# Performance work log

Hardware: AMD Instinct MI355X
Metric: run time of the kernel (lower is better)

## Reference

```python
import math
import jax, jax.numpy as jnp
import numpy as np

N_LAYERS = 30
RC = 64        # residual_channels
N_MELS = 80
TED = 128      # time_emb_dim
CD = 256       # text_dim
B, T = 8, 8192
EPS = 1e-12    # F.normalize eps


def conv1d(x, w, b, dilation=1, padding=0):
    # x: [B,C,T], w: [O,I,K], b: [O]
    y = jax.lax.conv_general_dilated(
        x, w, window_strides=(1,), padding=[(padding, padding)],
        rhs_dilation=(dilation,), dimension_numbers=("NCH", "OIH", "NCH"))
    return y + b[None, :, None]


def sinusoidal_embedding(t, dim):
    half = dim // 2
    freqs = jnp.exp(jnp.arange(half, dtype=jnp.float32) * (-math.log(10000.0) / (half - 1)))
    ang = t.astype(jnp.float32)[:, None] * freqs[None, :]
    return jnp.concatenate([jnp.sin(ang), jnp.cos(ang)], axis=1)  # [B, dim]


def mish(x):
    return x * jnp.tanh(jax.nn.softplus(x))


def setup_inputs() -> dict:
    key = jax.random.key(0)
    ks = jax.random.split(key, 24)
    s = 0.05
    inp = {
        "x": jax.random.normal(ks[0], (B, 1, N_MELS, T), jnp.float32),
        "t": jax.random.randint(ks[1], (B,), 0, 1000),
        "c_emb": jax.random.normal(ks[2], (B, CD), jnp.float32),
        # input_proj: Conv1d(n_mels, RC, 1)
        "in_w": jax.random.normal(ks[3], (RC, N_MELS, 1), jnp.float32) * s,
        "in_b": jnp.zeros((RC,), jnp.float32),
        # time MLP: Linear(TED, 4*TED), Mish, Linear(4*TED, TED). torch weight [out,in]
        "te_w1": jax.random.normal(ks[4], (4 * TED, TED), jnp.float32) * s,
        "te_b1": jnp.zeros((4 * TED,), jnp.float32),
        "te_w2": jax.random.normal(ks[5], (TED, 4 * TED), jnp.float32) * s,
        "te_b2": jnp.zeros((TED,), jnp.float32),
        # per-layer stacked params
        "dconv_w": jax.random.normal(ks[6], (N_LAYERS, 2 * RC, RC, 3), jnp.float32) * s,
        "dconv_b": jnp.zeros((N_LAYERS, 2 * RC), jnp.float32),
        "tproj_w": jax.random.normal(ks[7], (N_LAYERS, 2 * RC, TED), jnp.float32) * s,
        "tproj_b": jnp.zeros((N_LAYERS, 2 * RC), jnp.float32),
        "cproj_w": jax.random.normal(ks[8], (N_LAYERS, 2 * RC, CD), jnp.float32) * s,
        "cproj_b": jnp.zeros((N_LAYERS, 2 * RC), jnp.float32),
        "rs_w": jax.random.normal(ks[9], (N_LAYERS, 2 * RC, RC, 1), jnp.float32) * s,
        "rs_b": jnp.zeros((N_LAYERS, 2 * RC), jnp.float32),
        "skip_w": jax.random.normal(ks[10], (RC, RC, 1), jnp.float32) * s,
        "skip_b": jnp.zeros((RC,), jnp.float32),
        "out_w": jax.random.normal(ks[11], (N_MELS, RC, 1), jnp.float32) * s,
        "out_b": jnp.zeros((N_MELS,), jnp.float32),
    }
    return inp


def reference(x, t, c_emb, in_w, in_b, te_w1, te_b1, te_w2, te_b2,
              dconv_w, dconv_b, tproj_w, tproj_b, cproj_w, cproj_b,
              rs_w, rs_b, skip_w, skip_b, out_w, out_b):
    h = x[:, 0]                                  # squeeze(1) -> [B, n_mels, T]
    h = conv1d(h, in_w, in_b)                    # [B, RC, T]
    te = sinusoidal_embedding(t, TED)
    te = mish(te @ te_w1.T + te_b1) @ te_w2.T + te_b2   # [B, TED]

    skips = jnp.zeros_like(conv1d(h, rs_w[0], rs_b[0])[:, :RC])  # [B, RC, T]
    skips = jnp.zeros((h.shape[0], RC, h.shape[2]), h.dtype)
    for i in range(N_LAYERS):
        dil = 2 ** (i % 10)
        g = conv1d(h, dconv_w[i], dconv_b[i], dilation=dil, padding=dil)  # [B, 2RC, T]
        tp = (te @ tproj_w[i].T + tproj_b[i])[:, :, None]                 # [B, 2RC, 1]
        tp = tp / jnp.maximum(jnp.abs(tp), EPS)      # F.normalize over size-1 dim
        cp = (c_emb @ cproj_w[i].T + cproj_b[i])[:, :, None]
        cp = cp / jnp.maximum(jnp.abs(cp), EPS)
        g = g + tp + cp
        gate, filt = g[:, :RC], g[:, RC:]            # chunk(2, dim=1)
        out = jnp.tanh(filt) * jax.nn.sigmoid(gate)
        rs = conv1d(out, rs_w[i], rs_b[i])           # [B, 2RC, T]
        res, skip = rs[:, :RC], rs[:, RC:]
        h = h + res * (1.0 / math.sqrt(2.0))
        skips = skips + skip

    y = skips / math.sqrt(N_LAYERS)
    y = jax.nn.relu(conv1d(y, skip_w, skip_b))
    y = conv1d(y, out_w, out_b)                      # [B, n_mels, T]
    return y[:, None]                                # unsqueeze(1)
```

## Files before the change

kernel.cpp:

```cpp
#include <hip/hip_runtime.h>
#include <hip/hip_bf16.h>
#include <math.h>

#define NL 30
#define NM 80
#define Bx 8
#define Tx 8192

typedef short short8 __attribute__((ext_vector_type(8)));
typedef float f32x4 __attribute__((ext_vector_type(4)));
typedef unsigned int u32x2 __attribute__((ext_vector_type(2)));
typedef unsigned int u32x4 __attribute__((ext_vector_type(4)));

__device__ __forceinline__ float bf2f(unsigned short u) {
    union { unsigned int u; float f; } v; v.u = ((unsigned int)u) << 16; return v.f;
}
__device__ __forceinline__ unsigned short f2bf(float f) {
    union { float f; unsigned int u; } v; v.f = f;
    unsigned int r = v.u + 0x7FFFu + ((v.u >> 16) & 1u);
    return (unsigned short)(r >> 16);
}

#if defined(__has_builtin)
#if __has_builtin(__builtin_amdgcn_global_load_lds)
#define HAS_GLL 1
#endif
#endif

__device__ __forceinline__ void gll16(const void* g, void* l) {
#ifdef HAS_GLL
    __builtin_amdgcn_global_load_lds(
        (const __attribute__((address_space(1))) void*)g,
        (__attribute__((address_space(3))) void*)l, 16, 0, 0);
#else
    int lane = threadIdx.x & 63;
    *(u32x4*)((char*)l + lane * 16) = *(const u32x4*)((const char*)g + lane * 16);
#endif
}

__global__ __launch_bounds__(512) void setup_kernel(
        const float* __restrict__ dconv_w, const float* __restrict__ rs_w,
        const float* __restrict__ skip_w, const float* __restrict__ out_w,
        unsigned short* __restrict__ wc2, unsigned short* __restrict__ wr2,
        unsigned short* __restrict__ skw16, unsigned short* __restrict__ oww16,
        const float* __restrict__ x, const float* __restrict__ in_w,
        const float* __restrict__ in_b, unsigned short* __restrict__ h0) {
    __shared__ __align__(16) unsigned char smem[49152];
    int blk = blockIdx.x;
    int tid = threadIdx.x;
    if (blk < 30) {
        int l = blk;
        unsigned short* st = (unsigned short*)smem;
        const f32x4* src4 = (const f32x4*)(dconv_w + (size_t)l * 24576);
        #pragma unroll
        for (int h = 0; h < 2; ++h) {
            f32x4 v[6];
            #pragma unroll
            for (int it = 0; it < 6; ++it)
                v[it] = src4[(h * 6 + it) * 512 + tid];
            #pragma unroll
            for (int it = 0; it < 6; ++it) {
                int chunk = (h * 6 + it) * 512 + tid;
                #pragma unroll
                for (int e = 0; e < 4; ++e) {
                    int sidx = chunk * 4 + e;
                    int oc = sidx / 192;
                    int r = sidx - oc * 192;
                    int ic = r / 3;
                    int tap = r - ic * 3;
                    int dst = tap * 8192 + oc * 64 + (((ic >> 3) ^ (oc & 7)) << 3) + (ic & 7);
                    st[dst] = f2bf(v[it][e]);
                }
            }
        }
        __syncthreads();
        u32x4* dst4 = (u32x4*)(wc2 + (size_t)l * 24576);
        const u32x4* s4 = (const u32x4*)st;
        #pragma unroll
        for (int it = 0; it < 6; ++it)
            dst4[it * 512 + tid] = s4[it * 512 + tid];
    } else if (blk < 60) {
        int l = blk - 30;
        unsigned short* st = (unsigned short*)smem;
        const f32x4* src4 = (const f32x4*)(rs_w + (size_t)l * 8192);
        f32x4 v[4];
        #pragma unroll
        for (int it = 0; it < 4; ++it)
            v[it] = src4[it * 512 + tid];
        #pragma unroll
        for (int it = 0; it < 4; ++it) {
            int chunk = it * 512 + tid;
            #pragma unroll
            for (int e = 0; e < 4; ++e) {
                int sidx = chunk * 4 + e;
                int row = sidx >> 6;
                int ic = sidx & 63;
                int dst = row * 64 + (((ic >> 3) ^ (row & 7)) << 3) + (ic & 7);
                st[dst] = f2bf(v[it][e]);
            }
        }
        __syncthreads();
        u32x4* dst4 = (u32x4*)(wr2 + (size_t)l * 8192);
        const u32x4* s4 = (const u32x4*)st;
        #pragma unroll
        for (int it = 0; it < 2; ++it)
            dst4[it * 512 + tid] = s4[it * 512 + tid];
    } else if (blk == 60) {
        for (int j = tid; j < 4096; j += 512)
            skw16[j] = f2bf(skip_w[j] * 0.18257418583505536f);
        for (int j = tid; j < 5120; j += 512)
            oww16[j] = f2bf(out_w[j]);
    } else {
        float (*wT)[64] = (float(*)[64])smem;
        for (int i = tid; i < NM * 64; i += 512) {
            int m = i >> 6, c = i & 63;
            wT[m][c] = in_w[c * NM + m];
        }
        __syncthreads();
        int j = blk - 61;
        int b = j >> 5;
        int t = (j & 31) * 256 + (tid >> 1);
        int ch0 = (tid & 1) * 32;
        const float* xp = x + (size_t)b * NM * Tx + t;
        float acc[32];
        #pragma unroll
        for (int c = 0; c < 32; ++c) acc[c] = in_b[ch0 + c];
        #pragma unroll 1
        for (int m0 = 0; m0 < NM; m0 += 8) {
            float xv[8];
            #pragma unroll
            for (int u = 0; u < 8; ++u) xv[u] = xp[(size_t)(m0 + u) * Tx];
            #pragma unroll
            for (int u = 0; u < 8; ++u) {
                #pragma unroll
                for (int c = 0; c < 32; ++c)
                    acc[c] = fmaf(xv[u], wT[m0 + u][ch0 + c], acc[c]);
            }
        }
        unsigned short* hp = h0 + ((size_t)b * Tx + t) * 64 + ch0;
        #pragma unroll
        for (int c = 0; c < 32; c += 2) {
            unsigned int p = (unsigned int)f2bf(acc[c]) | ((unsigned int)f2bf(acc[c + 1]) << 16);
            *(unsigned int*)(hp + c) = p;
        }
    }
}

__global__ __launch_bounds__(512) void gbias_kernel(
        const int* __restrict__ tin,
        const float* __restrict__ w1, const float* __restrict__ b1,
        const float* __restrict__ w2, const float* __restrict__ b2,
        const float* __restrict__ cemb,
        const float* __restrict__ tpw, const float* __restrict__ tpb,
        const float* __restrict__ cpw, const float* __restrict__ cpb,
        const float* __restrict__ dcb,
        float* __restrict__ gbias) {
    __shared__ float emb[128];
    __shared__ float h1s[512];
    __shared__ float red[512];
    __shared__ float ted[128];
    int l = blockIdx.x >> 3;
    int b = blockIdx.x & 7;
    int tid = threadIdx.x, wid = tid >> 6, lane = tid & 63;

    if (tid < 64) {
        float fr = expf(-(float)tid * (logf(10000.f) / 63.f));
        float ang = (float)tin[b] * fr;
        emb[tid] = sinf(ang);
        emb[tid + 64] = cosf(ang);
    }
    __syncthreads();
    {
        float a = b1[tid];
        const f32x4* wr4 = (const f32x4*)(w1 + tid * 128);
        #pragma unroll 8
        for (int k = 0; k < 32; ++k) {
            f32x4 w4 = wr4[k];
            a = fmaf(emb[k * 4], w4[0], a);
            a = fmaf(emb[k * 4 + 1], w4[1], a);
            a = fmaf(emb[k * 4 + 2], w4[2], a);
            a = fmaf(emb[k * 4 + 3], w4[3], a);
        }
        float sp = (a > 15.f) ? a : log1pf(expf(a));
        h1s[tid] = a * tanhf(sp);
    }
    __syncthreads();
    {
        int o = tid & 127, q = tid >> 7;
        float p = 0.f;
        const f32x4* wr4 = (const f32x4*)(w2 + o * 512 + q * 128);
        const float* hq = h1s + q * 128;
        #pragma unroll 8
        for (int k = 0; k < 32; ++k) {
            f32x4 w4 = wr4[k];
            p = fmaf(hq[k * 4], w4[0], p);
            p = fmaf(hq[k * 4 + 1], w4[1], p);
            p = fmaf(hq[k * 4 + 2], w4[2], p);
            p = fmaf(hq[k * 4 + 3], w4[3], p);
        }
        red[tid] = p;
    }
    __syncthreads();
    if (tid < 128)
        ted[tid] = b2[tid] + red[tid] + red[tid + 128] + red[tid + 256] + red[tid + 384];
    __syncthreads();

    float te0 = ted[lane];
    float te1 = ted[64 + lane];
    float ce0 = cemb[b * 256 + lane];
    float ce1 = cemb[b * 256 + 64 + lane];
    float ce2 = cemb[b * 256 + 128 + lane];
    float ce3 = cemb[b * 256 + 192 + lane];
    #pragma unroll 4
    for (int i = 0; i < 16; ++i) {
        int ch = i * 8 + wid;
        const float* wr = tpw + (size_t)(l * 128 + ch) * 128;
        float s = te0 * wr[lane] + te1 * wr[lane + 64];
        const float* wc = cpw + (size_t)(l * 128 + ch) * 256;
        float sc = ce0 * wc[lane] + ce1 * wc[lane + 64] + ce2 * wc[lane + 128] + ce3 * wc[lane + 192];
        #pragma unroll
        for (int off = 32; off >= 1; off >>= 1) {
            s += __shfl_xor(s, off, 64);
            sc += __shfl_xor(sc, off, 64);
        }
        if (lane == 0) {
            float tp = tpb[l * 128 + ch] + s;
            float cp = cpb[l * 128 + ch] + sc;
            float s1 = tp / fmaxf(fabsf(tp), 1e-12f);
            float s2 = cp / fmaxf(fabsf(cp), 1e-12f);
            gbias[(l * 8 + b) * 128 + ch] = dcb[l * 128 + ch] + s1 + s2;
        }
    }
}

__launch_bounds__(512, 4)
__global__ void layer_kernel(const unsigned short* __restrict__ h_in,
                             unsigned short* __restrict__ h_out,
                             float* __restrict__ skips,
                             const unsigned short* __restrict__ wc2,
                             const unsigned short* __restrict__ wr2,
                             const float* __restrict__ gbias,
                             const float* __restrict__ rsb,
                             int dil, int first) {
    __shared__ __align__(16) unsigned char lds[81920];
    unsigned char* ldsA = lds;
    unsigned char* ldsR = lds + 49152;
    unsigned char* ldsO = lds + 65536;

    int tid = threadIdx.x;
    int wid = tid >> 6, lane = tid & 63, lr = lane & 15, lq = lane >> 4;

    #pragma unroll
    for (int j = 0; j < 6; ++j) {
        int cbase = j * 512 + wid * 64;
        gll16(wc2 + (size_t)(cbase + lane) * 8, ldsA + cbase * 16);
    }
    #pragma unroll
    for (int j = 0; j < 2; ++j) {
        int cbase = j * 512 + wid * 64;
        gll16(wr2 + (size_t)(cbase + lane) * 8, ldsR + cbase * 16);
    }

    int bid = blockIdx.x;
    int wg = (bid & 7) * 64 + (bid >> 3);
    int b = wg >> 6;
    int t0 = ((wg & 63) << 7) + wid * 16;

    const unsigned short* hb = h_in + (size_t)b * Tx * 64;
    short8 bv[3][2];
    #pragma unroll
    for (int tap = 0; tap < 3; ++tap) {
        int toff = (tap - 1) * dil;
        int t = t0 + lr + toff;
        bool v = ((unsigned)t < (unsigned)Tx);
        #pragma unroll
        for (int kc = 0; kc < 2; ++kc) {
            short8 z = {0, 0, 0, 0, 0, 0, 0, 0};
            if (v) z = *(const short8*)(hb + t * 64 + kc * 32 + lq * 8);
            bv[tap][kc] = z;
        }
    }

    f32x4 acc[8];
    #pragma unroll
    for (int mf = 0; mf < 8; ++mf)
        acc[mf] = *(const f32x4*)(gbias + b * 128 + mf * 16 + lq * 4);
    __syncthreads();

    #pragma unroll
    for (int tap = 0; tap < 3; ++tap) {
        #pragma unroll
        for (int kc = 0; kc < 2; ++kc) {
            #pragma unroll
            for (int mf = 0; mf < 8; ++mf) {
                int row = tap * 128 + mf * 16 + lr;
                short8 af = *(const short8*)(ldsA + row * 128 + ((kc * 64 + lq * 16) ^ ((lr & 7) << 4)));
                acc[mf] = __builtin_amdgcn_mfma_f32_16x16x32_bf16(af, bv[tap][kc], acc[mf], 0, 0, 0);
            }
        }
    }

    size_t base = ((size_t)b * Tx + t0 + lr) * 64;
    u32x2 hv[4];
    f32x4 sko[4];
    #pragma unroll
    for (int mf = 0; mf < 4; ++mf) {
        hv[mf] = *(const u32x2*)(h_in + base + mf * 16 + lq * 4);
        if (!first) sko[mf] = *(const f32x4*)(skips + base + mf * 16 + lq * 4);
        else { sko[mf][0] = 0.f; sko[mf][1] = 0.f; sko[mf][2] = 0.f; sko[mf][3] = 0.f; }
    }

    unsigned char* myO = ldsO + wid * 2048;
    #pragma unroll
    for (int mf = 0; mf < 4; ++mf) {
        int p = lr;
        unsigned short ob[4];
        #pragma unroll
        for (int r = 0; r < 4; ++r) {
            float g = acc[mf][r];
            float f = acc[mf + 4][r];
            f = fminf(f, 15.f);
            g = fminf(g, 30.f);
            float ea = __builtin_amdgcn_exp2f(f * 2.8853900817779268f);
            float eb = __builtin_amdgcn_exp2f(g * 1.4426950408889634f);
            float num = (ea - 1.f) * eb;
            float den = (ea + 1.f) * (1.f + eb);
            ob[r] = f2bf(num * __builtin_amdgcn_rcpf(den));
        }
        u32x2 pk;
        pk[0] = (unsigned int)ob[0] | ((unsigned int)ob[1] << 16);
        pk[1] = (unsigned int)ob[2] | ((unsigned int)ob[3] << 16);
        *(u32x2*)(myO + p * 128 + ((mf * 32 + lq * 8) ^ ((p & 7) << 4))) = pk;
    }

    const float rt2 = 1.41421356237309505f;
    f32x4 racc[8];
    #pragma unroll
    for (int mf = 0; mf < 4; ++mf) {
        f32x4 rb = *(const f32x4*)(rsb + mf * 16 + lq * 4);
        unsigned short* hp = (unsigned short*)&hv[mf];
        f32x4 r;
        #pragma unroll
        for (int r_ = 0; r_ < 4; ++r_) r[r_] = fmaf(bf2f(hp[r_]), rt2, rb[r_]);
        racc[mf] = r;
    }
    #pragma unroll
    for (int mf = 0; mf < 4; ++mf)
        racc[mf + 4] = *(const f32x4*)(rsb + 64 + mf * 16 + lq * 4) + sko[mf];

    #pragma unroll
    for (int kc = 0; kc < 2; ++kc) {
        int p = lr;
        short8 ov = *(const short8*)(myO + p * 128 + ((kc * 64 + lq * 16) ^ ((p & 7) << 4)));
        #pragma unroll
        for (int mf = 0; mf < 8; ++mf) {
            int row = mf * 16 + lr;
            short8 af = *(const short8*)(ldsR + row * 128 + ((kc * 64 + lq * 16) ^ ((lr & 7) << 4)));
            racc[mf] = __builtin_amdgcn_mfma_f32_16x16x32_bf16(af, ov, racc[mf], 0, 0, 0);
        }
    }

    const float inv_s2 = 0.70710678118654752f;
    #pragma unroll
    for (int mf = 0; mf < 4; ++mf) {
        unsigned short hnew[4];
        #pragma unroll
        for (int r = 0; r < 4; ++r)
            hnew[r] = f2bf(racc[mf][r] * inv_s2);
        u32x2 hw;
        hw[0] = (unsigned int)hnew[0] | ((unsigned int)hnew[1] << 16);
        hw[1] = (unsigned int)hnew[2] | ((unsigned int)hnew[3] << 16);
        *(u32x2*)(h_out + base + mf * 16 + lq * 4) = hw;
        *(f32x4*)(skips + base + mf * 16 + lq * 4) = racc[mf + 4];
    }
}

__launch_bounds__(512, 2)
__global__ void layer_last_kernel(const unsigned short* __restrict__ h_in,
                                  const float* __restrict__ skips,
                                  const unsigned short* __restrict__ wc2,
                                  const unsigned short* __restrict__ wr2,
                                  const float* __restrict__ gbias,
                                  const float* __restrict__ rsb,
                                  const unsigned short* __restrict__ skw,
                                  const float* __restrict__ skb,
                                  const unsigned short* __restrict__ oww,
                                  const float* __restrict__ obias,
                                  float* __restrict__ y,
                                  int dil) {
    __shared__ __align__(16) unsigned char lds[81920];
    unsigned char* ldsA = lds;
    unsigned char* ldsR = lds + 49152;
    unsigned char* ldsO = lds + 65536;

    int tid = threadIdx.x;
    int wid = tid >> 6, lane = tid & 63, lr = lane & 15, lq = lane >> 4;

    #pragma unroll
    for (int j = 0; j < 6; ++j) {
        int cbase = j * 512 + wid * 64;
        gll16(wc2 + (size_t)(cbase + lane) * 8, ldsA + cbase * 16);
    }
    #pragma unroll
    for (int j = 0; j < 2; ++j) {
        int cbase = j * 512 + wid * 64;
        gll16(wr2 + (size_t)(cbase + lane) * 8, ldsR + cbase * 16);
    }

    int bid = blockIdx.x;
    int wg = (bid & 7) * 64 + (bid >> 3);
    int b = wg >> 6;
    int t0 = ((wg & 63) << 7) + wid * 16;

    const unsigned short* hb = h_in + (size_t)b * Tx * 64;
    short8 bv[3][2];
    #pragma unroll
    for (int tap = 0; tap < 3; ++tap) {
        int toff = (tap - 1) * dil;
        int t = t0 + lr + toff;
        bool v = ((unsigned)t < (unsigned)Tx);
        #pragma unroll
        for (int kc = 0; kc < 2; ++kc) {
            short8 z = {0, 0, 0, 0, 0, 0, 0, 0};
            if (v) z = *(const short8*)(hb + t * 64 + kc * 32 + lq * 8);
            bv[tap][kc] = z;
        }
    }

    f32x4 acc[8];
    #pragma unroll
    for (int mf = 0; mf < 8; ++mf)
        acc[mf] = *(const f32x4*)(gbias + b * 128 + mf * 16 + lq * 4);
    __syncthreads();

    #pragma unroll
    for (int tap = 0; tap < 3; ++tap) {
        #pragma unroll
        for (int kc = 0; kc < 2; ++kc) {
            #pragma unroll
            for (int mf = 0; mf < 8; ++mf) {
                int row = tap * 128 + mf * 16 + lr;
                short8 af = *(const short8*)(ldsA + row * 128 + ((kc * 64 + lq * 16) ^ ((lr & 7) << 4)));
                acc[mf] = __builtin_amdgcn_mfma_f32_16x16x32_bf16(af, bv[tap][kc], acc[mf], 0, 0, 0);
            }
        }
    }

    size_t base = ((size_t)b * Tx + t0 + lr) * 64;
    f32x4 sko[4];
    #pragma unroll
    for (int mf = 0; mf < 4; ++mf)
        sko[mf] = *(const f32x4*)(skips + base + mf * 16 + lq * 4);

    unsigned char* myO = ldsO + wid * 2048;
    #pragma unroll
    for (int mf = 0; mf < 4; ++mf) {
        int p = lr;
        unsigned short ob[4];
        #pragma unroll
        for (int r = 0; r < 4; ++r) {
            float g = acc[mf][r];
            float f = acc[mf + 4][r];
            f = fminf(f, 15.f);
            g = fminf(g, 30.f);
            float ea = __builtin_amdgcn_exp2f(f * 2.8853900817779268f);
            float eb = __builtin_amdgcn_exp2f(g * 1.4426950408889634f);
            float num = (ea - 1.f) * eb;
            float den = (ea + 1.f) * (1.f + eb);
            ob[r] = f2bf(num * __builtin_amdgcn_rcpf(den));
        }
        u32x2 pk;
        pk[0] = (unsigned int)ob[0] | ((unsigned int)ob[1] << 16);
        pk[1] = (unsigned int)ob[2] | ((unsigned int)ob[3] << 16);
        *(u32x2*)(myO + p * 128 + ((mf * 32 + lq * 8) ^ ((p & 7) << 4))) = pk;
    }

    f32x4 racc[4];
    #pragma unroll
    for (int mf = 0; mf < 4; ++mf)
        racc[mf] = *(const f32x4*)(rsb + 64 + mf * 16 + lq * 4) + sko[mf];
    #pragma unroll
    for (int kc = 0; kc < 2; ++kc) {
        int p = lr;
        short8 ov = *(const short8*)(myO + p * 128 + ((kc * 64 + lq * 16) ^ ((p & 7) << 4)));
        #pragma unroll
        for (int mf = 0; mf < 4; ++mf) {
            int row = 64 + mf * 16 + lr;
            short8 af = *(const short8*)(ldsR + row * 128 + ((kc * 64 + lq * 16) ^ ((lr & 7) << 4)));
            racc[mf] = __builtin_amdgcn_mfma_f32_16x16x32_bf16(af, ov, racc[mf], 0, 0, 0);
        }
    }

    #pragma unroll
    for (int mf = 0; mf < 4; ++mf) {
        int p = lr;
        u32x2 pk;
        pk[0] = (unsigned int)f2bf(racc[mf][0]) | ((unsigned int)f2bf(racc[mf][1]) << 16);
        pk[1] = (unsigned int)f2bf(racc[mf][2]) | ((unsigned int)f2bf(racc[mf][3]) << 16);
        *(u32x2*)(myO + p * 128 + ((mf * 32 + lq * 8) ^ ((p & 7) << 4))) = pk;
    }

    f32x4 yacc[4];
    #pragma unroll
    for (int mf = 0; mf < 4; ++mf)
        yacc[mf] = *(const f32x4*)(skb + mf * 16 + lq * 4);
    #pragma unroll
    for (int kc = 0; kc < 2; ++kc) {
        int p = lr;
        short8 Bv = *(const short8*)(myO + p * 128 + ((kc * 64 + lq * 16) ^ ((p & 7) << 4)));
        #pragma unroll
        for (int mf = 0; mf < 4; ++mf) {
            short8 A1 = *(const short8*)(skw + (mf * 16 + lr) * 64 + kc * 32 + lq * 8);
            yacc[mf] = __builtin_amdgcn_mfma_f32_16x16x32_bf16(A1, Bv, yacc[mf], 0, 0, 0);
        }
    }
    #pragma unroll
    for (int mf = 0; mf < 4; ++mf) {
        int p = lr;
        u32x2 pk;
        pk[0] = (unsigned int)f2bf(fmaxf(yacc[mf][0], 0.f)) | ((unsigned int)f2bf(fmaxf(yacc[mf][1], 0.f)) << 16);
        pk[1] = (unsigned int)f2bf(fmaxf(yacc[mf][2], 0.f)) | ((unsigned int)f2bf(fmaxf(yacc[mf][3], 0.f)) << 16);
        *(u32x2*)(myO + p * 128 + ((mf * 32 + lq * 8) ^ ((p & 7) << 4))) = pk;
    }

    f32x4 oacc[5];
    #pragma unroll
    for (int mf = 0; mf < 5; ++mf)
        oacc[mf] = *(const f32x4*)(obias + mf * 16 + lq * 4);
    #pragma unroll
    for (int kc = 0; kc < 2; ++kc) {
        int p = lr;
        short8 B2 = *(const short8*)(myO + p * 128 + ((kc * 64 + lq * 16) ^ ((p & 7) << 4)));
        #pragma unroll
        for (int mf = 0; mf < 5; ++mf) {
            short8 A2 = *(const short8*)(oww + (mf * 16 + lr) * 64 + kc * 32 + lq * 8);
            oacc[mf] = __builtin_amdgcn_mfma_f32_16x16x32_bf16(A2, B2, oacc[mf], 0, 0, 0);
        }
    }
    int t = t0 + lr;
    #pragma unroll
    for (int mf = 0; mf < 5; ++mf) {
        #pragma unroll
        for (int r = 0; r < 4; ++r) {
            int m = mf * 16 + lq * 4 + r;
            y[((size_t)b * NM + m) * Tx + t] = oacc[mf][r];
        }
    }
}

extern "C" void kernel_launch(void* const* d_in, const int* in_sizes, int n_in,
                              void* d_out, int out_size, void* d_ws, size_t ws_size,
                              hipStream_t stream) {
    const float* x       = (const float*)d_in[0];
    const int*   tin     = (const int*)d_in[1];
    const float* c_emb   = (const float*)d_in[2];
    const float* in_w    = (const float*)d_in[3];
    const float* in_b    = (const float*)d_in[4];
    const float* te_w1   = (const float*)d_in[5];
    const float* te_b1   = (const float*)d_in[6];
    const float* te_w2   = (const float*)d_in[7];
    const float* te_b2   = (const float*)d_in[8];
    const float* dconv_w = (const float*)d_in[9];
    const float* dconv_b = (const float*)d_in[10];
    const float* tproj_w = (const float*)d_in[11];
    const float* tproj_b = (const float*)d_in[12];
    const float* cproj_w = (const float*)d_in[13];
    const float* cproj_b = (const float*)d_in[14];
    const float* rs_w    = (const float*)d_in[15];
    const float* rs_b    = (const float*)d_in[16];
    const float* skip_w  = (const float*)d_in[17];
    const float* skip_b  = (const float*)d_in[18];
    const float* out_w   = (const float*)d_in[19];
    const float* out_b   = (const float*)d_in[20];

    char* ws = (char*)d_ws;
    float* gbias          = (float*)(ws + 4096);
    unsigned short* skw16 = (unsigned short*)(ws + 126976);
    unsigned short* oww16 = (unsigned short*)(ws + 135168);
    unsigned short* wc2   = (unsigned short*)(ws + 145408);
    unsigned short* wr2   = (unsigned short*)(ws + 1619968);
    unsigned short* h0    = (unsigned short*)(ws + 2111488);
    unsigned short* h1    = (unsigned short*)(ws + 10500096);
    float* skips          = (float*)(ws + 18888704);

    setup_kernel<<<317, 512, 0, stream>>>(dconv_w, rs_w, skip_w, out_w,
                                          wc2, wr2, skw16, oww16,
                                          x, in_w, in_b, h0);
    gbias_kernel<<<240, 512, 0, stream>>>(tin, te_w1, te_b1, te_w2, te_b2,
                                          c_emb, tproj_w, tproj_b,
                                          cproj_w, cproj_b, dconv_b, gbias);

    unsigned short* hin = h0;
    unsigned short* hout = h1;
    for (int i = 0; i < NL - 1; ++i) {
        int dil = 1 << (i % 10);
        layer_kernel<<<512, 512, 0, stream>>>(hin, hout, skips,
                                              wc2 + (size_t)i * 24576,
                                              wr2 + (size_t)i * 8192,
                                              gbias + (size_t)i * 1024,
                                              rs_b + (size_t)i * 128,
                                              dil, i == 0 ? 1 : 0);
        unsigned short* tmp = hin; hin = hout; hout = tmp;
    }
    layer_last_kernel<<<512, 512, 0, stream>>>(hin, skips,
                                               wc2 + (size_t)(NL - 1) * 24576,
                                               wr2 + (size_t)(NL - 1) * 8192,
                                               gbias + (size_t)(NL - 1) * 1024,
                                               rs_b + (size_t)(NL - 1) * 128,
                                               skw16, skip_b, oww16, out_b,
                                               (float*)d_out, 1 << ((NL - 1) % 10));
}
```

Measured before the change: 556.8 us.

## Fuse pairs of small-dilation layers into one kernel with halo recompute

Adds a layer_pair_kernel that runs two consecutive residual layers in one launch. It keeps the intermediate h in LDS and recomputes the first layer on halo tiles so the second layer's dilated conv has the neighbours it needs. It is used for the pairs whose second dilation is at most 32, which removes one global round-trip of h and skips plus one launch per pair. In exchange it recomputes halo tiles, uses more LDS (112 KB, so lower occupancy at launch_bounds 2), and adds an extra weight-staging phase with block-wide syncs.

```diff
diff --git a/kernel.cpp b/kernel.cpp
--- a/kernel.cpp
+++ b/kernel.cpp
@@ -36,6 +36,22 @@
     int lane = threadIdx.x & 63;
     *(u32x4*)((char*)l + lane * 16) = *(const u32x4*)((const char*)g + lane * 16);
 #endif
+}
+
+__device__ __forceinline__ void stageW(const unsigned short* __restrict__ wc,
+                                       const unsigned short* __restrict__ wr,
+                                       unsigned char* ldsA, unsigned char* ldsR, int tid) {
+    int w = tid >> 6, lane = tid & 63;
+    #pragma unroll
+    for (int j = 0; j < 6; ++j) {
+        int cbase = j * 512 + w * 64;
+        gll16(wc + (size_t)(cbase + lane) * 8, ldsA + cbase * 16);
+    }
+    #pragma unroll
+    for (int j = 0; j < 2; ++j) {
+        int cbase = j * 512 + w * 64;
+        gll16(wr + (size_t)(cbase + lane) * 8, ldsR + cbase * 16);
+    }
 }
 
 __global__ __launch_bounds__(512) void setup_kernel(
@@ -250,16 +266,7 @@
     int tid = threadIdx.x;
     int wid = tid >> 6, lane = tid & 63, lr = lane & 15, lq = lane >> 4;
 
-    #pragma unroll
-    for (int j = 0; j < 6; ++j) {
-        int cbase = j * 512 + wid * 64;
-        gll16(wc2 + (size_t)(cbase + lane) * 8, ldsA + cbase * 16);
-    }
-    #pragma unroll
-    for (int j = 0; j < 2; ++j) {
-        int cbase = j * 512 + wid * 64;
-        gll16(wr2 + (size_t)(cbase + lane) * 8, ldsR + cbase * 16);
-    }
+    stageW(wc2, wr2, ldsA, ldsR, tid);
 
     int bid = blockIdx.x;
     int wg = (bid & 7) * 64 + (bid >> 3);
@@ -372,6 +379,251 @@
         hw[1] = (unsigned int)hnew[2] | ((unsigned int)hnew[3] << 16);
         *(u32x2*)(h_out + base + mf * 16 + lq * 4) = hw;
         *(f32x4*)(skips + base + mf * 16 + lq * 4) = racc[mf + 4];
+    }
+}
+
+__launch_bounds__(512, 2)
+__global__ void layer_pair_kernel(const unsigned short* __restrict__ h_in,
+                                  unsigned short* __restrict__ h_out,
+                                  float* __restrict__ skips,
+                                  const unsigned short* __restrict__ wc2a,
+                                  const unsigned short* __restrict__ wr2a,
+                                  const float* __restrict__ gba,
+                                  const float* __restrict__ rsba,
+                                  int l1, int dil1, int dil2, int ht16, int first) {
+    __shared__ __align__(16) unsigned char lds[114688];
+    unsigned char* ldsA = lds;
+    unsigned char* ldsR = lds + 49152;
+    unsigned char* ldsH = lds + 65536;
+    unsigned char* ldsO = lds + 90112;
+
+    int tid = threadIdx.x;
+    int w = tid >> 6, lane = tid & 63, lr = lane & 15, lq = lane >> 4;
+    int l2 = l1 + 1;
+    const float rt2 = 1.41421356237309505f;
+    const float inv_s2 = 0.70710678118654752f;
+
+    stageW(wc2a + (size_t)l1 * 24576, wr2a + (size_t)l1 * 8192, ldsA, ldsR, tid);
+
+    int bid = blockIdx.x;
+    int wg = (bid & 7) * 64 + (bid >> 3);
+    int b = wg >> 6;
+    int t0 = (wg & 63) << 7;
+    int T = 8 + 2 * ht16;
+    int ct = (w >= ht16) ? w : 8 + w;
+
+    const unsigned short* hb = h_in + (size_t)b * Tx * 64;
+    const float* gb1 = gba + (size_t)(l1 * 8 + b) * 128;
+    const float* rsb1 = rsba + (size_t)l1 * 128;
+    __syncthreads();
+
+    for (int k = 0; k < 2; ++k) {
+        int tile = k ? 8 + w : w;
+        if (k && tile >= T) break;
+        int gtb = t0 + (tile - ht16) * 16;
+        short8 bv[3][2];
+        #pragma unroll
+        for (int tap = 0; tap < 3; ++tap) {
+            int t = gtb + lr + (tap - 1) * dil1;
+            bool v = ((unsigned)t < (unsigned)Tx);
+            #pragma unroll
+            for (int kc = 0; kc < 2; ++kc) {
+                short8 z = {0, 0, 0, 0, 0, 0, 0, 0};
+                if (v) z = *(const short8*)(hb + t * 64 + kc * 32 + lq * 8);
+                bv[tap][kc] = z;
+            }
+        }
+        f32x4 acc[8];
+        #pragma unroll
+        for (int mf = 0; mf < 8; ++mf)
+            acc[mf] = *(const f32x4*)(gb1 + mf * 16 + lq * 4);
+        #pragma unroll
+        for (int tap = 0; tap < 3; ++tap) {
+            #pragma unroll
+            for (int kc = 0; kc < 2; ++kc) {
+                #pragma unroll
+                for (int mf = 0; mf < 8; ++mf) {
+                    int row = tap * 128 + mf * 16 + lr;
+                    short8 af = *(const short8*)(ldsA + row * 128 + ((kc * 64 + lq * 16) ^ ((lr & 7) << 4)));
+                    acc[mf] = __builtin_amdgcn_mfma_f32_16x16x32_bf16(af, bv[tap][kc], acc[mf], 0, 0, 0);
+                }
+            }
+        }
+        unsigned char* myO = ldsO + tile * 2048;
+        #pragma unroll
+        for (int mf = 0; mf < 4; ++mf) {
+            int p = lr;
+            unsigned short ob[4];
+            #pragma unroll
+            for (int r = 0; r < 4; ++r) {
+                float g = acc[mf][r];
+                float f = acc[mf + 4][r];
+                f = fminf(f, 15.f);
+                g = fminf(g, 30.f);
+                float ea = __builtin_amdgcn_exp2f(f * 2.8853900817779268f);
+                float eb = __builtin_amdgcn_exp2f(g * 1.4426950408889634f);
+                float num = (ea - 1.f) * eb;
+                float den = (ea + 1.f) * (1.f + eb);
+                ob[r] = f2bf(num * __builtin_amdgcn_rcpf(den));
+            }
+            u32x2 pk;
+            pk[0] = (unsigned int)ob[0] | ((unsigned int)ob[1] << 16);
+            pk[1] = (unsigned int)ob[2] | ((unsigned int)ob[3] << 16);
+            *(u32x2*)(myO + p * 128 + ((mf * 32 + lq * 8) ^ ((p & 7) << 4))) = pk;
+        }
+    }
+
+    f32x4 sk1[4];
+    u32x2 hn1[4];
+    for (int k = 0; k < 2; ++k) {
+        int tile = k ? 8 + w : w;
+        if (k && tile >= T) break;
+        int gtb = t0 + (tile - ht16) * 16;
+        int t = gtb + lr;
+        bool tv = ((unsigned)t < (unsigned)Tx);
+        u32x2 hv[4];
+        #pragma unroll
+        for (int mf = 0; mf < 4; ++mf) {
+            u32x2 z; z[0] = 0u; z[1] = 0u;
+            if (tv) z = *(const u32x2*)(h_in + ((size_t)b * Tx + t) * 64 + mf * 16 + lq * 4);
+            hv[mf] = z;
+        }
+        f32x4 racc[8];
+        #pragma unroll
+        for (int mf = 0; mf < 4; ++mf) {
+            f32x4 rb = *(const f32x4*)(rsb1 + mf * 16 + lq * 4);
+            unsigned short* hp = (unsigned short*)&hv[mf];
+            f32x4 r;
+            #pragma unroll
+            for (int r_ = 0; r_ < 4; ++r_) r[r_] = fmaf(bf2f(hp[r_]), rt2, rb[r_]);
+            racc[mf] = r;
+        }
+        #pragma unroll
+        for (int mf = 0; mf < 4; ++mf)
+            racc[mf + 4] = *(const f32x4*)(rsb1 + 64 + mf * 16 + lq * 4);
+        unsigned char* myO = ldsO + tile * 2048;
+        #pragma unroll
+        for (int kc = 0; kc < 2; ++kc) {
+            int p = lr;
+            short8 ov = *(const short8*)(myO + p * 128 + ((kc * 64 + lq * 16) ^ ((p & 7) << 4)));
+            #pragma unroll
+            for (int mf = 0; mf < 8; ++mf) {
+                int row = mf * 16 + lr;
+                short8 af = *(const short8*)(ldsR + row * 128 + ((kc * 64 + lq * 16) ^ ((lr & 7) << 4)));
+                racc[mf] = __builtin_amdgcn_mfma_f32_16x16x32_bf16(af, ov, racc[mf], 0, 0, 0);
+            }
+        }
+        int hrow = tile * 16 + lr;
+        #pragma unroll
+        for (int mf = 0; mf < 4; ++mf) {
+            u32x2 pk; pk[0] = 0u; pk[1] = 0u;
+            if (tv) {
+                unsigned short hn[4];
+                #pragma unroll
+                for (int r = 0; r < 4; ++r)
+                    hn[r] = f2bf(racc[mf][r] * inv_s2);
+                pk[0] = (unsigned int)hn[0] | ((unsigned int)hn[1] << 16);
+                pk[1] = (unsigned int)hn[2] | ((unsigned int)hn[3] << 16);
+            }
+            *(u32x2*)(ldsH + hrow * 128 + ((mf * 32 + lq * 8) ^ ((hrow & 7) << 4))) = pk;
+            if (tile == ct) { sk1[mf] = racc[mf + 4]; hn1[mf] = pk; }
+        }
+    }
+    __syncthreads();
+
+    stageW(wc2a + (size_t)l2 * 24576, wr2a + (size_t)l2 * 8192, ldsA, ldsR, tid);
+    int gtc = t0 + (ct - ht16) * 16;
+    size_t cbase = ((size_t)b * Tx + gtc + lr) * 64;
+    f32x4 sko[4];
+    #pragma unroll
+    for (int mf = 0; mf < 4; ++mf) {
+        if (!first) sko[mf] = *(const f32x4*)(skips + cbase + mf * 16 + lq * 4);
+        else { sko[mf][0] = 0.f; sko[mf][1] = 0.f; sko[mf][2] = 0.f; sko[mf][3] = 0.f; }
+    }
+    const float* gb2 = gba + (size_t)(l2 * 8 + b) * 128;
+    const float* rsb2 = rsba + (size_t)l2 * 128;
+    f32x4 acc2[8];
+    #pragma unroll
+    for (int mf = 0; mf < 8; ++mf)
+        acc2[mf] = *(const f32x4*)(gb2 + mf * 16 + lq * 4);
+    __syncthreads();
+
+    int lrow0 = ct * 16 + lr;
+    #pragma unroll
+    for (int tap = 0; tap < 3; ++tap) {
+        int row = lrow0 + (tap - 1) * dil2;
+        #pragma unroll
+        for (int kc = 0; kc < 2; ++kc) {
+            short8 bv2 = *(const short8*)(ldsH + row * 128 + ((kc * 64 + lq * 16) ^ ((row & 7) << 4)));
+            #pragma unroll
+            for (int mf = 0; mf < 8; ++mf) {
+                int wrow = tap * 128 + mf * 16 + lr;
+                short8 af = *(const short8*)(ldsA + wrow * 128 + ((kc * 64 + lq * 16) ^ ((lr & 7) << 4)));
+                acc2[mf] = __builtin_amdgcn_mfma_f32_16x16x32_bf16(af, bv2, acc2[mf], 0, 0, 0);
+            }
+        }
+    }
+
+    unsigned char* myO = ldsO + ct * 2048;
+    #pragma unroll
+    for (int mf = 0; mf < 4; ++mf) {
+        int p = lr;
+        unsigned short ob[4];
+        #pragma unroll
+        for (int r = 0; r < 4; ++r) {
+            float g = acc2[mf][r];
+            float f = acc2[mf + 4][r];
+            f = fminf(f, 15.f);
+            g = fminf(g, 30.f);
+            float ea = __builtin_amdgcn_exp2f(f * 2.8853900817779268f);
+            float eb = __builtin_amdgcn_exp2f(g * 1.4426950408889634f);
+            float num = (ea - 1.f) * eb;
+            float den = (ea + 1.f) * (1.f + eb);
+            ob[r] = f2bf(num * __builtin_amdgcn_rcpf(den));
+        }
+        u32x2 pk;
+        pk[0] = (unsigned int)ob[0] | ((unsigned int)ob[1] << 16);
+        pk[1] = (unsigned int)ob[2] | ((unsigned int)ob[3] << 16);
+        *(u32x2*)(myO + p * 128 + ((mf * 32 + lq * 8) ^ ((p & 7) << 4))) = pk;
+    }
+
+    f32x4 racc2[8];
+    #pragma unroll
+    for (int mf = 0; mf < 4; ++mf) {
+        f32x4 rb = *(const f32x4*)(rsb2 + mf * 16 + lq * 4);
+        unsigned short* hp = (unsigned short*)&hn1[mf];
+        f32x4 r;
+        #pragma unroll
+        for (int r_ = 0; r_ < 4; ++r_) r[r_] = fmaf(bf2f(hp[r_]), rt2, rb[r_]);
+        racc2[mf] = r;
+    }
+    #pragma unroll
+    for (int mf = 0; mf < 4; ++mf)
+        racc2[mf + 4] = *(const f32x4*)(rsb2 + 64 + mf * 16 + lq * 4) + sko[mf] + sk1[mf];
+
+    #pragma unroll
+    for (int kc = 0; kc < 2; ++kc) {
+        int p = lr;
+        short8 ov = *(const short8*)(myO + p * 128 + ((kc * 64 + lq * 16) ^ ((p & 7) << 4)));
+        #pragma unroll
+        for (int mf = 0; mf < 8; ++mf) {
+            int row = mf * 16 + lr;
+            short8 af = *(const short8*)(ldsR + row * 128 + ((kc * 64 + lq * 16) ^ ((lr & 7) << 4)));
+            racc2[mf] = __builtin_amdgcn_mfma_f32_16x16x32_bf16(af, ov, racc2[mf], 0, 0, 0);
+        }
+    }
+
+    #pragma unroll
+    for (int mf = 0; mf < 4; ++mf) {
+        unsigned short hnew[4];
+        #pragma unroll
+        for (int r = 0; r < 4; ++r)
+            hnew[r] = f2bf(racc2[mf][r] * inv_s2);
+        u32x2 hw;
+        hw[0] = (unsigned int)hnew[0] | ((unsigned int)hnew[1] << 16);
+        hw[1] = (unsigned int)hnew[2] | ((unsigned int)hnew[3] << 16);
+        *(u32x2*)(h_out + cbase + mf * 16 + lq * 4) = hw;
+        *(f32x4*)(skips + cbase + mf * 16 + lq * 4) = racc2[mf + 4];
     }
 }
 
@@ -396,16 +648,7 @@
     int tid = threadIdx.x;
     int wid = tid >> 6, lane = tid & 63, lr = lane & 15, lq = lane >> 4;
 
-    #pragma unroll
-    for (int j = 0; j < 6; ++j) {
-        int cbase = j * 512 + wid * 64;
-        gll16(wc2 + (size_t)(cbase + lane) * 8, ldsA + cbase * 16);
-    }
-    #pragma unroll
-    for (int j = 0; j < 2; ++j) {
-        int cbase = j * 512 + wid * 64;
-        gll16(wr2 + (size_t)(cbase + lane) * 8, ldsR + cbase * 16);
-    }
+    stageW(wc2, wr2, ldsA, ldsR, tid);
 
     int bid = blockIdx.x;
     int wg = (bid & 7) * 64 + (bid >> 3);
@@ -590,17 +833,34 @@
                                           c_emb, tproj_w, tproj_b,
                                           cproj_w, cproj_b, dconv_b, gbias);
 
+    bool pstart[29] = {false};
+    pstart[0] = pstart[2] = pstart[4] = pstart[9] = pstart[11] = pstart[13]
+              = pstart[19] = pstart[21] = pstart[23] = true;
+
     unsigned short* hin = h0;
     unsigned short* hout = h1;
-    for (int i = 0; i < NL - 1; ++i) {
+    int i = 0;
+    while (i < NL - 1) {
         int dil = 1 << (i % 10);
-        layer_kernel<<<512, 512, 0, stream>>>(hin, hout, skips,
-                                              wc2 + (size_t)i * 24576,
-                                              wr2 + (size_t)i * 8192,
-                                              gbias + (size_t)i * 1024,
-                                              rs_b + (size_t)i * 128,
-                                              dil, i == 0 ? 1 : 0);
-        unsigned short* tmp = hin; hin = hout; hout = tmp;
+        if (pstart[i]) {
+            int dil2 = 1 << ((i + 1) % 10);
+            int ht16 = (dil2 > 16) ? 2 : 1;
+            layer_pair_kernel<<<512, 512, 0, stream>>>(hin, hout, skips,
+                                                       wc2, wr2, gbias, rs_b,
+                                                       i, dil, dil2, ht16,
+                                                       i == 0 ? 1 : 0);
+            unsigned short* tmp = hin; hin = hout; hout = tmp;
+            i += 2;
+        } else {
+            layer_kernel<<<512, 512, 0, stream>>>(hin, hout, skips,
+                                                  wc2 + (size_t)i * 24576,
+                                                  wr2 + (size_t)i * 8192,
+                                                  gbias + (size_t)i * 1024,
+                                                  rs_b + (size_t)i * 128,
+                                                  dil, 0);
+            unsigned short* tmp = hin; hin = hout; hout = tmp;
+            i += 1;
+        }
     }
     layer_last_kernel<<<512, 512, 0, stream>>>(hin, skips,
                                                wc2 + (size_t)(NL - 1) * 24576,
```

After: 531.8 us. 4.5% less time.
